# Performance work log

Measured on AMD Instinct MI355X. Metric: run time of the kernel, lower is better.

The kernel has to match this reference:

```python
import jax, jax.numpy as jnp
import numpy as np

DIM = 1024
HEADS = 16
DH = 64            # dim // heads
LOCAL_HEADS = 8
WINDOW = 128
NEG = -jnp.finfo(jnp.float32).max


def _look_around_kv(z, pad_value):
    # z: (b, h, nw, w, d) -> (b, h, nw, 3w, d); backward=1, forward=1 window
    nw = z.shape[2]
    zp = jnp.pad(z, ((0, 0), (0, 0), (1, 1), (0, 0), (0, 0)), constant_values=pad_value)
    return jnp.concatenate([zp[:, :, i:i + nw] for i in range(3)], axis=3)


def _local_attention(q, k, v, valid):
    # q,k,v: (b, h, t, d); valid: (b, t) True = keep (module passes ~input_mask)
    b, h, t, d = q.shape
    nw = t // WINDOW
    bucket = lambda z: z.reshape(b, h, nw, WINDOW, d)
    bq, bk, bv = bucket(q), bucket(k), bucket(v)
    bk = _look_around_kv(bk, 0.0)
    bv = _look_around_kv(bv, 0.0)
    # key position indices with -1 padding for out-of-range windows
    t_idx = jnp.arange(t, dtype=jnp.int32).reshape(nw, WINDOW)
    tp = jnp.pad(t_idx, ((1, 1), (0, 0)), constant_values=-1)
    bq_k = jnp.concatenate([tp[i:i + nw] for i in range(3)], axis=1)  # (nw, 3w)
    oob = (bq_k == -1)[None, None, :, None, :]                        # (1,1,nw,1,3w)
    # input mask pair: mq & mk
    vm = valid.reshape(b, nw, WINDOW)
    vmp = jnp.pad(vm, ((0, 0), (1, 1), (0, 0)), constant_values=False)
    vmk = jnp.concatenate([vmp[:, i:i + nw] for i in range(3)], axis=2)  # (b, nw, 3w)
    pair = vm[:, None, :, :, None] & vmk[:, None, :, None, :]            # (b,1,nw,w,3w)
    dots = jnp.einsum('bhnwd,bhnkd->bhnwk', bq, bk) * (d ** -0.5)
    dots = jnp.where(oob, NEG, dots)
    dots = jnp.where(pair, dots, NEG)
    attn = jax.nn.softmax(dots, axis=-1)
    out = jnp.einsum('bhnwk,bhnkd->bhnwd', attn, bv)
    return out.reshape(b, h, t, d)


def _linear_attn(q, k, v, valid):
    # q,k,v: (b, h, t, d); valid: (b, t) True = keep
    d = q.shape[-1]
    m = valid[:, None, :, None]
    k = jnp.where(m, k, NEG)
    v = jnp.where(m, v, 0.0)
    q = jax.nn.softmax(q, axis=-1) * (d ** -0.5)
    k = jax.nn.softmax(k, axis=-2)
    context = jnp.einsum('bhnd,bhne->bhde', k, v)
    return jnp.einsum('bhnd,bhde->bhne', q, context)


def setup_inputs() -> dict:
    key = jax.random.key(0)
    ks = jax.random.split(key, 7)
    b, t = 2, 4096
    x = jax.random.normal(ks[0], (b, t, DIM), dtype=jnp.float32)
    input_mask = jax.random.bernoulli(ks[1], 0.1, (b, t))  # True = padded token
    s = DIM ** -0.5
    Wq = jax.random.normal(ks[2], (DIM, HEADS * DH), jnp.float32) * s
    Wk = jax.random.normal(ks[3], (DIM, HEADS * DH), jnp.float32) * s
    Wv = jax.random.normal(ks[4], (DIM, HEADS * DH), jnp.float32) * s
    Wo = jax.random.normal(ks[5], (HEADS * DH, DIM), jnp.float32) * s
    bo = jax.random.normal(ks[6], (DIM,), jnp.float32) * 0.01
    return {"x": x, "input_mask": input_mask, "Wq": Wq, "Wk": Wk, "Wv": Wv, "Wo": Wo, "bo": bo}


def reference(x, input_mask, Wq, Wk, Wv, Wo, bo):
    b, t, _ = x.shape
    split_heads = lambda z: z.reshape(b, t, HEADS, DH).transpose(0, 2, 1, 3)
    q = split_heads(x @ Wq)
    k = split_heads(x @ Wk)
    v = split_heads(x @ Wv)
    valid = ~input_mask
    lq, gq = q[:, :LOCAL_HEADS], q[:, LOCAL_HEADS:]
    lk, gk = k[:, :LOCAL_HEADS], k[:, LOCAL_HEADS:]
    lv, gv = v[:, :LOCAL_HEADS], v[:, LOCAL_HEADS:]
    local_out = _local_attention(lq, lk, lv, valid)
    global_out = _linear_attn(gq, gk, gv, valid)
    attn = jnp.concatenate([local_out, global_out], axis=1)  # (b, h, t, d)
    attn = attn.transpose(0, 2, 1, 3).reshape(b, t, HEADS * DH)
    return attn @ Wo + bo
```

## Files before the change

kernel.cpp:

```cpp
#include <hip/hip_runtime.h>
#include <cstdint>
#include <cfloat>
#include <math.h>

typedef __bf16 bf16_t;
typedef __bf16 bf16x8 __attribute__((ext_vector_type(8)));
typedef __bf16 bf16x4 __attribute__((ext_vector_type(4)));
typedef float  f32x4  __attribute__((ext_vector_type(4)));

#define NEGF (-3.4028234663852886e38f)

static __device__ __forceinline__ f32x4 mfma16(bf16x8 a, bf16x8 b, f32x4 c) {
  return __builtin_amdgcn_mfma_f32_16x16x32_bf16(a, b, c, 0, 0, 0);
}
static __device__ __forceinline__ void gload_lds16(const bf16_t* g, bf16_t* l) {
  __builtin_amdgcn_global_load_lds((const __attribute__((address_space(1))) void*)g,
                                   (__attribute__((address_space(3))) void*)l, 16, 0, 0);
}

__global__ void k_prep(const uint8_t* __restrict__ mraw, uint8_t* __restrict__ valid) {
  __shared__ int f1, f3;
  int tid = threadIdx.x;
  if (tid == 0) { f1 = 0; f3 = 0; }
  __syncthreads();
  int l1 = 0, l3 = 0;
  for (int i = tid; i < 8192; i += 256) {
    uint8_t v = mraw[i];
    if (v) { int r = i & 3; if (r == 1 || r == 2) l1 = 1; if (r == 3) l3 = 1; }
  }
  if (l1) atomicOr(&f1, 1);
  if (l3) atomicOr(&f3, 1);
  __syncthreads();
  int layout = f1 ? 0 : (f3 ? 2 : 1);
  for (int i = tid; i < 8192; i += 256) {
    bool m;
    if (layout == 0)      m = mraw[i] != 0;
    else if (layout == 1) m = ((const int*)mraw)[i] != 0;
    else                  m = ((const float*)mraw)[i] != 0.0f;
    valid[i] = m ? (uint8_t)0 : (uint8_t)1;
  }
}

__global__ void k_cast_x(const float* __restrict__ x, bf16_t* __restrict__ xb) {
  int i = blockIdx.x * 256 + threadIdx.x;
  float4 v = ((const float4*)x)[i];
  bf16x4 o = { (bf16_t)v.x, (bf16_t)v.y, (bf16_t)v.z, (bf16_t)v.w };
  *(bf16x4*)(xb + (size_t)i * 4) = o;
}

__global__ void k_transw(const float* __restrict__ Wq, const float* __restrict__ Wk,
                         const float* __restrict__ Wv, const float* __restrict__ Wo,
                         bf16_t* __restrict__ WT, bf16_t* __restrict__ WoT) {
  __shared__ float tile[32][33];
  int z = blockIdx.z;
  const float* src = (z == 0) ? Wq : (z == 1) ? Wk : (z == 2) ? Wv : Wo;
  bf16_t* dst = (z < 3) ? (WT + (size_t)z * 1024 * 1024) : WoT;
  int x0 = blockIdx.x * 32, y0 = blockIdx.y * 32;
  int tx = threadIdx.x, ty = threadIdx.y;
  #pragma unroll
  for (int j = 0; j < 32; j += 8)
    tile[ty + j][tx] = src[(size_t)(y0 + ty + j) * 1024 + x0 + tx];
  __syncthreads();
  #pragma unroll
  for (int j = 0; j < 32; j += 8)
    dst[(size_t)(x0 + ty + j) * 1024 + y0 + tx] = (bf16_t)tile[tx][ty + j];
}

template<bool OUT_BF16>
__global__ __launch_bounds__(256, 2) void k_gemm(const bf16_t* __restrict__ A,
                                                 const bf16_t* __restrict__ Bt,
                                                 void* __restrict__ Cout,
                                                 const float* __restrict__ bias,
                                                 int M, int N, int K) {
  __shared__ __align__(16) uint8_t shmem[34816];
  bf16_t* As = (bf16_t*)shmem;
  bf16_t* Bs = As + 128 * 64;
  int nbn = N >> 7;
  int nwg = (M >> 7) * nbn;
  int per = nwg >> 3;
  int id  = blockIdx.x;
  int sw  = (id & 7) * per + (id >> 3);
  int mb = sw / nbn, nb = sw % nbn;

  const int tid = threadIdx.x;
  const int lane = tid & 63, wv = tid >> 6;
  const int c = lane & 15, g = lane >> 4;
  const size_t m0 = (size_t)mb * 128, n0 = (size_t)nb * 128;
  const int wm = (wv >> 1) * 64, wn = (wv & 1) * 64;

  f32x4 zero = {0.f, 0.f, 0.f, 0.f};
  f32x4 acc[4][4];
  #pragma unroll
  for (int m = 0; m < 4; ++m)
    #pragma unroll
    for (int n = 0; n < 4; ++n) acc[m][n] = zero;

  for (int kt = 0; kt < K; kt += 64) {
    if (kt) __syncthreads();
    #pragma unroll
    for (int p = 0; p < 4; ++p) {
      int seg = p * 256 + tid;
      int r = seg >> 3, s = seg & 7;
      int sc = (s ^ (r & 7)) * 8;
      gload_lds16(A + (m0 + r) * (size_t)K + kt + sc, As + seg * 8);
    }
    #pragma unroll
    for (int p = 0; p < 4; ++p) {
      int seg = p * 256 + tid;
      int r = seg >> 3, s = seg & 7;
      int sc = (s ^ (r & 7)) * 8;
      gload_lds16(Bt + (n0 + r) * (size_t)K + kt + sc, Bs + seg * 8);
    }
    __syncthreads();
    #pragma unroll
    for (int kk = 0; kk < 2; ++kk) {
      bf16x8 af[4], bfv[4];
      #pragma unroll
      for (int m = 0; m < 4; ++m) {
        int row = wm + m * 16 + c;
        int sl = (g + 4 * kk) ^ (row & 7);
        af[m] = *(const bf16x8*)(As + row * 64 + sl * 8);
      }
      #pragma unroll
      for (int n = 0; n < 4; ++n) {
        int row = wn + n * 16 + c;
        int sl = (g + 4 * kk) ^ (row & 7);
        bfv[n] = *(const bf16x8*)(Bs + row * 64 + sl * 8);
      }
      #pragma unroll
      for (int m = 0; m < 4; ++m)
        #pragma unroll
        for (int n = 0; n < 4; ++n)
          acc[m][n] = mfma16(af[m], bfv[n], acc[m][n]);
    }
  }

  __syncthreads();
  if (OUT_BF16) {
    bf16_t* L = (bf16_t*)shmem;
    #pragma unroll
    for (int m = 0; m < 4; ++m)
      #pragma unroll
      for (int n = 0; n < 4; ++n)
        #pragma unroll
        for (int i = 0; i < 4; ++i)
          L[(wm + m * 16 + 4 * g + i) * 136 + wn + n * 16 + c] = (bf16_t)acc[m][n][i];
    __syncthreads();
    bf16_t* C = (bf16_t*)Cout;
    #pragma unroll
    for (int p = 0; p < 8; ++p) {
      int idx = p * 2048 + tid * 8;
      int row = idx >> 7, col = idx & 127;
      bf16x8 v = *(const bf16x8*)(L + row * 136 + col);
      *(bf16x8*)(C + (m0 + row) * (size_t)N + n0 + col) = v;
    }
  } else {
    float* C = (float*)Cout;
    float* L = (float*)shmem;
    #pragma unroll
    for (int half = 0; half < 2; ++half) {
      if (half) __syncthreads();
      if ((wv >> 1) == half) {
        #pragma unroll
        for (int m = 0; m < 4; ++m)
          #pragma unroll
          for (int n = 0; n < 4; ++n)
            #pragma unroll
            for (int i = 0; i < 4; ++i)
              L[(m * 16 + 4 * g + i) * 132 + wn + n * 16 + c] = acc[m][n][i];
      }
      __syncthreads();
      #pragma unroll
      for (int p = 0; p < 8; ++p) {
        int lin = p * 1024 + tid * 4;
        int row = lin >> 7, col = lin & 127;
        float4 v = *(const float4*)(L + row * 132 + col);
        float4 bv = *(const float4*)(bias + n0 + col);
        v.x += bv.x; v.y += bv.y; v.z += bv.z; v.w += bv.w;
        *(float4*)(C + (m0 + half * 64 + row) * (size_t)N + n0 + col) = v;
      }
    }
  }
}

__global__ __launch_bounds__(512) void k_local(const bf16_t* __restrict__ qkv,
                                               const uint8_t* __restrict__ valid,
                                               bf16_t* __restrict__ attn) {
  __shared__ __align__(16) uint8_t smem[151040];
  bf16_t* Ks = (bf16_t*)smem;
  bf16_t* P  = (bf16_t*)smem;
  bf16_t* VT = (bf16_t*)(smem + 100352);
  uint8_t* s_key = smem + 150528;
  uint8_t* s_q   = smem + 150912;

  int bid = blockIdx.x;
  int w = bid & 31, h = (bid >> 5) & 7, b = bid >> 8;
  int tid = threadIdx.x;
  const int lane = tid & 63, wv = tid >> 6;
  const int c = lane & 15, g = lane >> 4;
  const int tkbase = (w - 1) * 128;

  #pragma unroll
  for (int p = 0; p < 6; ++p) {
    int seg = p * 512 + tid;
    int r = seg >> 3, s = seg & 7;
    int tk = tkbase + r;
    bf16x8 v8 = { (bf16_t)0.f,(bf16_t)0.f,(bf16_t)0.f,(bf16_t)0.f,
                  (bf16_t)0.f,(bf16_t)0.f,(bf16_t)0.f,(bf16_t)0.f };
    if ((unsigned)tk < 4096u)
      v8 = *(const bf16x8*)(qkv + (size_t)(b * 4096 + tk) * 3072 + 1024 + h * 64 + s * 8);
    *(bf16x8*)(Ks + r * 64 + ((s ^ (r & 7)) * 8)) = v8;
  }
  {
    int e = tid & 63, tg = tid >> 6;
    #pragma unroll 8
    for (int j = 0; j < 48; ++j) {
      int r = tg * 48 + j;
      int tk = tkbase + r;
      bf16_t v = (bf16_t)0.f;
      if ((unsigned)tk < 4096u)
        v = qkv[(size_t)(b * 4096 + tk) * 3072 + 2048 + h * 64 + e];
      VT[e * 392 + r] = v;
    }
  }
  if (tid < 384) {
    int tk = tkbase + tid;
    s_key[tid] = ((unsigned)tk < 4096u) ? valid[b * 4096 + tk] : (uint8_t)0;
  }
  if (tid < 128) s_q[tid] = valid[b * 4096 + w * 128 + tid];
  __syncthreads();

  int m0 = wv * 16;
  bf16x8 qa0, qa1;
  {
    const bf16_t* qrow = qkv + (size_t)(b * 4096 + w * 128 + m0 + c) * 3072 + h * 64;
    qa0 = *(const bf16x8*)(qrow + g * 8);
    qa1 = *(const bf16x8*)(qrow + 32 + g * 8);
  }
  f32x4 zero = {0.f, 0.f, 0.f, 0.f};
  f32x4 acc[24];
  #pragma unroll
  for (int nt = 0; nt < 24; ++nt) acc[nt] = zero;
  #pragma unroll
  for (int nt = 0; nt < 24; ++nt) {
    int n = nt * 16 + c;
    bf16x8 b0 = *(const bf16x8*)(Ks + n * 64 + ((g       ^ (n & 7)) * 8));
    bf16x8 b1 = *(const bf16x8*)(Ks + n * 64 + (((g + 4) ^ (n & 7)) * 8));
    acc[nt] = mfma16(qa0, b0, acc[nt]);
    acc[nt] = mfma16(qa1, b1, acc[nt]);
  }

  bool qv[4];
  #pragma unroll
  for (int i = 0; i < 4; ++i) qv[i] = s_q[m0 + 4 * g + i] != 0;
  #pragma unroll
  for (int nt = 0; nt < 24; ++nt) {
    bool kv = s_key[nt * 16 + c] != 0;
    #pragma unroll
    for (int i = 0; i < 4; ++i)
      acc[nt][i] = (kv && qv[i]) ? acc[nt][i] * 0.125f : NEGF;
  }
  float mx[4], sum[4];
  #pragma unroll
  for (int i = 0; i < 4; ++i) mx[i] = NEGF;
  #pragma unroll
  for (int nt = 0; nt < 24; ++nt)
    #pragma unroll
    for (int i = 0; i < 4; ++i) mx[i] = fmaxf(mx[i], acc[nt][i]);
  #pragma unroll
  for (int sh = 1; sh <= 8; sh <<= 1)
    #pragma unroll
    for (int i = 0; i < 4; ++i) mx[i] = fmaxf(mx[i], __shfl_xor(mx[i], sh, 64));
  #pragma unroll
  for (int i = 0; i < 4; ++i) sum[i] = 0.f;
  #pragma unroll
  for (int nt = 0; nt < 24; ++nt)
    #pragma unroll
    for (int i = 0; i < 4; ++i) {
      float e = __expf(acc[nt][i] - mx[i]);
      acc[nt][i] = e;
      sum[i] += e;
    }
  #pragma unroll
  for (int sh = 1; sh <= 8; sh <<= 1)
    #pragma unroll
    for (int i = 0; i < 4; ++i) sum[i] += __shfl_xor(sum[i], sh, 64);
  float inv[4];
  #pragma unroll
  for (int i = 0; i < 4; ++i) inv[i] = 1.f / sum[i];

  __syncthreads();
  #pragma unroll
  for (int nt = 0; nt < 24; ++nt)
    #pragma unroll
    for (int i = 0; i < 4; ++i)
      P[(m0 + 4 * g + i) * 392 + nt * 16 + c] = (bf16_t)(acc[nt][i] * inv[i]);
  __syncthreads();

  f32x4 o[4];
  #pragma unroll
  for (int n = 0; n < 4; ++n) o[n] = zero;
  #pragma unroll
  for (int ks = 0; ks < 12; ++ks) {
    bf16x8 pa = *(const bf16x8*)(P + (m0 + c) * 392 + ks * 32 + g * 8);
    #pragma unroll
    for (int n = 0; n < 4; ++n) {
      bf16x8 vb = *(const bf16x8*)(VT + (n * 16 + c) * 392 + ks * 32 + g * 8);
      o[n] = mfma16(pa, vb, o[n]);
    }
  }
  size_t obase = (size_t)(b * 4096 + w * 128 + m0) * 1024 + h * 64;
  #pragma unroll
  for (int n = 0; n < 4; ++n)
    #pragma unroll
    for (int i = 0; i < 4; ++i)
      attn[obase + (size_t)(4 * g + i) * 1024 + n * 16 + c] = (bf16_t)o[n][i];
}

__global__ __launch_bounds__(256) void k_ctx1(const bf16_t* __restrict__ qkv,
                                              const uint8_t* __restrict__ valid,
                                              float* __restrict__ ctxp,
                                              float* __restrict__ sump) {
  int bid = blockIdx.x;
  int tc = bid & 15, h = (bid >> 4) & 7, b = bid >> 7;
  int tid = threadIdx.x;
  __shared__ float sk[128][64];
  __shared__ float sv[128][64];
  float a00=0,a01=0,a02=0,a03=0,a10=0,a11=0,a12=0,a13=0;
  float a20=0,a21=0,a22=0,a23=0,a30=0,a31=0,a32=0,a33=0;
  float s0=0, s1=0, s2=0, s3=0;
  int dg = tid >> 4, eg = tid & 15;
  for (int ch = 0; ch < 2; ++ch) {
    int t0 = tc * 256 + ch * 128;
    __syncthreads();
    for (int idx = tid; idx < 1024; idx += 256) {
      int r = idx >> 3, ss = idx & 7;
      int gt = b * 4096 + t0 + r;
      bool vld = valid[gt] != 0;
      bf16x8 k8 = *(const bf16x8*)(qkv + (size_t)gt * 3072 + 1024 + (8 + h) * 64 + ss * 8);
      bf16x8 v8 = *(const bf16x8*)(qkv + (size_t)gt * 3072 + 2048 + (8 + h) * 64 + ss * 8);
      #pragma unroll
      for (int j = 0; j < 8; ++j) {
        int dd = ss * 8 + j;
        sk[r][dd] = vld ? __expf((float)k8[j]) : 0.f;
        sv[r][dd] = vld ? (float)v8[j] : 0.f;
      }
    }
    __syncthreads();
    #pragma unroll 4
    for (int r = 0; r < 128; ++r) {
      float4 a = *(const float4*)&sk[r][dg * 4];
      float4 v = *(const float4*)&sv[r][eg * 4];
      a00 += a.x*v.x; a01 += a.x*v.y; a02 += a.x*v.z; a03 += a.x*v.w;
      a10 += a.y*v.x; a11 += a.y*v.y; a12 += a.y*v.z; a13 += a.y*v.w;
      a20 += a.z*v.x; a21 += a.z*v.y; a22 += a.z*v.z; a23 += a.z*v.w;
      a30 += a.w*v.x; a31 += a.w*v.y; a32 += a.w*v.z; a33 += a.w*v.w;
      s0 += a.x; s1 += a.y; s2 += a.z; s3 += a.w;
    }
  }
  float* dst = ctxp + (size_t)((b * 8 + h) * 16 + tc) * 4096 + (dg * 4) * 64 + eg * 4;
  *(float4*)(dst + 0)   = make_float4(a00, a01, a02, a03);
  *(float4*)(dst + 64)  = make_float4(a10, a11, a12, a13);
  *(float4*)(dst + 128) = make_float4(a20, a21, a22, a23);
  *(float4*)(dst + 192) = make_float4(a30, a31, a32, a33);
  if (eg == 0)
    *(float4*)(sump + (size_t)((b * 8 + h) * 16 + tc) * 64 + dg * 4) = make_float4(s0, s1, s2, s3);
}

__global__ __launch_bounds__(256) void k_ctx2(const float* __restrict__ ctxp,
                                              const float* __restrict__ sump,
                                              bf16_t* __restrict__ ctxT) {
  int bh = blockIdx.x;
  int tid = threadIdx.x;
  __shared__ float inv[64];
  if (tid < 64) {
    float s = 0.f;
    #pragma unroll
    for (int tc = 0; tc < 16; ++tc)
      s += sump[(size_t)(bh * 16 + tc) * 64 + tid];
    inv[tid] = 1.f / s;
  }
  __syncthreads();
  for (int p = 0; p < 16; ++p) {
    int lin = p * 256 + tid;
    int d = lin >> 6, e = lin & 63;
    float s = 0.f;
    #pragma unroll
    for (int tc = 0; tc < 16; ++tc)
      s += ctxp[(size_t)(bh * 16 + tc) * 4096 + lin];
    s *= inv[d];
    ctxT[(size_t)bh * 4096 + e * 64 + d] = (bf16_t)s;
  }
}

__global__ __launch_bounds__(256) void k_linout(const bf16_t* __restrict__ qkv,
                                                const bf16_t* __restrict__ ctxT,
                                                bf16_t* __restrict__ attn) {
  int bid = blockIdx.x;
  int tb2 = bid & 15, hg = (bid >> 4) & 7, b = bid >> 7;
  int tid = threadIdx.x;
  __shared__ bf16_t qs[256 * 72];
  __shared__ bf16_t cT[64 * 72];
  {
    int t = tb2 * 256 + tid;
    const bf16_t* qrow = qkv + (size_t)(b * 4096 + t) * 3072 + (8 + hg) * 64;
    float x[64];
    #pragma unroll
    for (int s8 = 0; s8 < 8; ++s8) {
      bf16x8 q8 = *(const bf16x8*)(qrow + s8 * 8);
      #pragma unroll
      for (int j = 0; j < 8; ++j) x[s8 * 8 + j] = (float)q8[j];
    }
    float m = x[0];
    #pragma unroll
    for (int i = 1; i < 64; ++i) m = fmaxf(m, x[i]);
    float sum = 0.f;
    #pragma unroll
    for (int i = 0; i < 64; ++i) { x[i] = __expf(x[i] - m); sum += x[i]; }
    float sc = 0.125f / sum;
    #pragma unroll
    for (int s8 = 0; s8 < 8; ++s8) {
      bf16x8 o8;
      #pragma unroll
      for (int j = 0; j < 8; ++j) o8[j] = (bf16_t)(x[s8 * 8 + j] * sc);
      *(bf16x8*)(qs + tid * 72 + s8 * 8) = o8;
    }
  }
  for (int idx = tid; idx < 512; idx += 256) {
    int r = idx >> 3, s = idx & 7;
    *(bf16x8*)(cT + r * 72 + s * 8) =
      *(const bf16x8*)(ctxT + (size_t)(b * 8 + hg) * 4096 + r * 64 + s * 8);
  }
  __syncthreads();
  int lane = tid & 63, wvv = tid >> 6;
  int c = lane & 15, g = lane >> 4;
  int m0w = wvv * 64;
  f32x4 zero = {0.f, 0.f, 0.f, 0.f};
  f32x4 acc[4][4];
  #pragma unroll
  for (int m = 0; m < 4; ++m)
    #pragma unroll
    for (int n = 0; n < 4; ++n) acc[m][n] = zero;
  #pragma unroll
  for (int kk = 0; kk < 2; ++kk) {
    bf16x8 af[4], bfv[4];
    #pragma unroll
    for (int m = 0; m < 4; ++m)
      af[m] = *(const bf16x8*)(qs + (m0w + m * 16 + c) * 72 + kk * 32 + g * 8);
    #pragma unroll
    for (int n = 0; n < 4; ++n)
      bfv[n] = *(const bf16x8*)(cT + (n * 16 + c) * 72 + kk * 32 + g * 8);
    #pragma unroll
    for (int m = 0; m < 4; ++m)
      #pragma unroll
      for (int n = 0; n < 4; ++n)
        acc[m][n] = mfma16(af[m], bfv[n], acc[m][n]);
  }
  size_t obase = (size_t)(b * 4096 + tb2 * 256 + m0w) * 1024 + (8 + hg) * 64;
  #pragma unroll
  for (int m = 0; m < 4; ++m)
    #pragma unroll
    for (int n = 0; n < 4; ++n)
      #pragma unroll
      for (int i = 0; i < 4; ++i)
        attn[obase + (size_t)(m * 16 + 4 * g + i) * 1024 + n * 16 + c] = (bf16_t)acc[m][n][i];
}

extern "C" void kernel_launch(void* const* d_in, const int* in_sizes, int n_in,
                              void* d_out, int out_size, void* d_ws, size_t ws_size,
                              hipStream_t stream) {
  const float*   x    = (const float*)d_in[0];
  const uint8_t* mraw = (const uint8_t*)d_in[1];
  const float*   Wq   = (const float*)d_in[2];
  const float*   Wk   = (const float*)d_in[3];
  const float*   Wv   = (const float*)d_in[4];
  const float*   Wo   = (const float*)d_in[5];
  const float*   bo   = (const float*)d_in[6];
  uint8_t* ws = (uint8_t*)d_ws;

  uint8_t* valid = ws;
  bf16_t*  xb    = (bf16_t*)(ws + 8192);
  bf16_t*  WT    = (bf16_t*)(ws + 16785408);
  bf16_t*  WoT   = (bf16_t*)(ws + 23076864);
  bf16_t*  qkv   = (bf16_t*)(ws + 25174016);
  bf16_t*  attn  = (bf16_t*)(ws + 75505664);
  float*   ctxp  = (float*)(ws + 8192);
  float*   sump  = (float*)(ws + 4202496);
  bf16_t*  ctxT  = (bf16_t*)(ws + 4268032);

  k_prep<<<1, 256, 0, stream>>>(mraw, valid);
  k_cast_x<<<8192, 256, 0, stream>>>(x, xb);
  k_transw<<<dim3(32, 32, 4), dim3(32, 8), 0, stream>>>(Wq, Wk, Wv, Wo, WT, WoT);
  k_gemm<true><<<1536, 256, 0, stream>>>(xb, WT, (void*)qkv, nullptr, 8192, 3072, 1024);
  k_local<<<512, 512, 0, stream>>>(qkv, valid, attn);
  k_ctx1<<<256, 256, 0, stream>>>(qkv, valid, ctxp, sump);
  k_ctx2<<<16, 256, 0, stream>>>(ctxp, sump, ctxT);
  k_linout<<<256, 256, 0, stream>>>(qkv, ctxT, attn);
  k_gemm<false><<<512, 256, 0, stream>>>(attn, WoT, d_out, bo, 8192, 1024, 1024);
}
```

Before: 220.2 us.

## Keep local-attention probabilities in registers and shrink shared memory

The local attention kernel now computes S^T by swapping the MFMA operands, so each lane holds one query row's scores. The softmax reduction then needs only two cross-lane shuffles. The probabilities are moved into A-operand layout with register shuffles instead of a round trip through shared memory. Normalisation is deferred to the output write, and K and V^T share one LDS buffer. This cuts LDS from about 151KB to about 50KB, which may let more blocks run per CU. The cost is more shuffles and register pressure (12 uint4 held per lane), and the V^T load is now serialized after QK^T.

Result: no change. 218.8 us (-0.7%).

```diff
diff --git a/kernel.cpp b/kernel.cpp
--- a/kernel.cpp
+++ b/kernel.cpp
@@ -7,6 +7,7 @@
 typedef __bf16 bf16x8 __attribute__((ext_vector_type(8)));
 typedef __bf16 bf16x4 __attribute__((ext_vector_type(4)));
 typedef float  f32x4  __attribute__((ext_vector_type(4)));
+typedef unsigned int u32;
 
 #define NEGF (-3.4028234663852886e38f)
 
@@ -186,12 +187,11 @@
 __global__ __launch_bounds__(512) void k_local(const bf16_t* __restrict__ qkv,
                                                const uint8_t* __restrict__ valid,
                                                bf16_t* __restrict__ attn) {
-  __shared__ __align__(16) uint8_t smem[151040];
+  __shared__ __align__(16) uint8_t smem[50688];
   bf16_t* Ks = (bf16_t*)smem;
-  bf16_t* P  = (bf16_t*)smem;
-  bf16_t* VT = (bf16_t*)(smem + 100352);
-  uint8_t* s_key = smem + 150528;
-  uint8_t* s_q   = smem + 150912;
+  bf16_t* VT = (bf16_t*)smem;
+  uint8_t* s_key = smem + 50176;
+  uint8_t* s_q   = smem + 50560;
 
   int bid = blockIdx.x;
   int w = bid & 31, h = (bid >> 5) & 7, b = bid >> 8;
@@ -211,6 +211,34 @@
       v8 = *(const bf16x8*)(qkv + (size_t)(b * 4096 + tk) * 3072 + 1024 + h * 64 + s * 8);
     *(bf16x8*)(Ks + r * 64 + ((s ^ (r & 7)) * 8)) = v8;
   }
+  if (tid < 384) {
+    int tk = tkbase + tid;
+    s_key[tid] = ((unsigned)tk < 4096u) ? valid[b * 4096 + tk] : (uint8_t)0;
+  }
+  if (tid < 128) s_q[tid] = valid[b * 4096 + w * 128 + tid];
+  __syncthreads();
+
+  int m0 = wv * 16;
+  bf16x8 qa0, qa1;
+  {
+    const bf16_t* qrow = qkv + (size_t)(b * 4096 + w * 128 + m0 + c) * 3072 + h * 64;
+    qa0 = *(const bf16x8*)(qrow + g * 8);
+    qa1 = *(const bf16x8*)(qrow + 32 + g * 8);
+  }
+  f32x4 zero = {0.f, 0.f, 0.f, 0.f};
+  f32x4 acc[24];
+  #pragma unroll
+  for (int nt = 0; nt < 24; ++nt) acc[nt] = zero;
+  #pragma unroll
+  for (int nt = 0; nt < 24; ++nt) {
+    int n = nt * 16 + c;
+    bf16x8 k0 = *(const bf16x8*)(Ks + n * 64 + ((g       ^ (n & 7)) * 8));
+    bf16x8 k1 = *(const bf16x8*)(Ks + n * 64 + (((g + 4) ^ (n & 7)) * 8));
+    acc[nt] = mfma16(k0, qa0, acc[nt]);
+    acc[nt] = mfma16(k1, qa1, acc[nt]);
+  }
+  __syncthreads();
+
   {
     int e = tid & 63, tg = tid >> 6;
     #pragma unroll 8
@@ -223,78 +251,59 @@
       VT[e * 392 + r] = v;
     }
   }
-  if (tid < 384) {
-    int tk = tkbase + tid;
-    s_key[tid] = ((unsigned)tk < 4096u) ? valid[b * 4096 + tk] : (uint8_t)0;
-  }
-  if (tid < 128) s_q[tid] = valid[b * 4096 + w * 128 + tid];
-  __syncthreads();
-
-  int m0 = wv * 16;
-  bf16x8 qa0, qa1;
-  {
-    const bf16_t* qrow = qkv + (size_t)(b * 4096 + w * 128 + m0 + c) * 3072 + h * 64;
-    qa0 = *(const bf16x8*)(qrow + g * 8);
-    qa1 = *(const bf16x8*)(qrow + 32 + g * 8);
-  }
-  f32x4 zero = {0.f, 0.f, 0.f, 0.f};
-  f32x4 acc[24];
-  #pragma unroll
-  for (int nt = 0; nt < 24; ++nt) acc[nt] = zero;
+
+  bool qv = s_q[m0 + c] != 0;
   #pragma unroll
   for (int nt = 0; nt < 24; ++nt) {
-    int n = nt * 16 + c;
-    bf16x8 b0 = *(const bf16x8*)(Ks + n * 64 + ((g       ^ (n & 7)) * 8));
-    bf16x8 b1 = *(const bf16x8*)(Ks + n * 64 + (((g + 4) ^ (n & 7)) * 8));
-    acc[nt] = mfma16(qa0, b0, acc[nt]);
-    acc[nt] = mfma16(qa1, b1, acc[nt]);
-  }
-
-  bool qv[4];
-  #pragma unroll
-  for (int i = 0; i < 4; ++i) qv[i] = s_q[m0 + 4 * g + i] != 0;
+    u32 kv4 = *(const u32*)(s_key + nt * 16 + 4 * g);
+    #pragma unroll
+    for (int i = 0; i < 4; ++i) {
+      bool kv = ((kv4 >> (8 * i)) & 255u) != 0u;
+      acc[nt][i] = (qv && kv) ? acc[nt][i] * 0.125f : NEGF;
+    }
+  }
+  float mx = NEGF;
+  #pragma unroll
+  for (int nt = 0; nt < 24; ++nt)
+    #pragma unroll
+    for (int i = 0; i < 4; ++i) mx = fmaxf(mx, acc[nt][i]);
+  mx = fmaxf(mx, __shfl_xor(mx, 16, 64));
+  mx = fmaxf(mx, __shfl_xor(mx, 32, 64));
+
+  const int srcA = ((lane >> 4) & 1) * 32 + (lane & 15);
+  const int srcB = srcA + 16;
+  union Pk2 { bf16x4 h; uint2 u; };
+  union Pk4 { uint4 u; bf16x8 h; };
+  uint4 paU[12];
+  #pragma unroll
+  for (int ks = 0; ks < 12; ++ks) paU[ks] = make_uint4(0, 0, 0, 0);
+  float sum = 0.f;
   #pragma unroll
   for (int nt = 0; nt < 24; ++nt) {
-    bool kv = s_key[nt * 16 + c] != 0;
-    #pragma unroll
-    for (int i = 0; i < 4; ++i)
-      acc[nt][i] = (kv && qv[i]) ? acc[nt][i] * 0.125f : NEGF;
-  }
-  float mx[4], sum[4];
-  #pragma unroll
-  for (int i = 0; i < 4; ++i) mx[i] = NEGF;
-  #pragma unroll
-  for (int nt = 0; nt < 24; ++nt)
-    #pragma unroll
-    for (int i = 0; i < 4; ++i) mx[i] = fmaxf(mx[i], acc[nt][i]);
-  #pragma unroll
-  for (int sh = 1; sh <= 8; sh <<= 1)
-    #pragma unroll
-    for (int i = 0; i < 4; ++i) mx[i] = fmaxf(mx[i], __shfl_xor(mx[i], sh, 64));
-  #pragma unroll
-  for (int i = 0; i < 4; ++i) sum[i] = 0.f;
-  #pragma unroll
-  for (int nt = 0; nt < 24; ++nt)
+    Pk2 pk;
     #pragma unroll
     for (int i = 0; i < 4; ++i) {
-      float e = __expf(acc[nt][i] - mx[i]);
-      acc[nt][i] = e;
-      sum[i] += e;
-    }
-  #pragma unroll
-  for (int sh = 1; sh <= 8; sh <<= 1)
-    #pragma unroll
-    for (int i = 0; i < 4; ++i) sum[i] += __shfl_xor(sum[i], sh, 64);
-  float inv[4];
-  #pragma unroll
-  for (int i = 0; i < 4; ++i) inv[i] = 1.f / sum[i];
-
-  __syncthreads();
-  #pragma unroll
-  for (int nt = 0; nt < 24; ++nt)
-    #pragma unroll
-    for (int i = 0; i < 4; ++i)
-      P[(m0 + 4 * g + i) * 392 + nt * 16 + c] = (bf16_t)(acc[nt][i] * inv[i]);
+      float e = __expf(acc[nt][i] - mx);
+      sum += e;
+      pk.h[i] = (bf16_t)e;
+    }
+    u32 a0 = (u32)__shfl((int)pk.u.x, srcA, 64);
+    u32 a1 = (u32)__shfl((int)pk.u.y, srcA, 64);
+    u32 b0 = (u32)__shfl((int)pk.u.x, srcB, 64);
+    u32 b1 = (u32)__shfl((int)pk.u.y, srcB, 64);
+    bool take = ((g >> 1) == (nt & 1));
+    int ks = nt >> 1;
+    paU[ks].x = take ? a0 : paU[ks].x;
+    paU[ks].y = take ? a1 : paU[ks].y;
+    paU[ks].z = take ? b0 : paU[ks].z;
+    paU[ks].w = take ? b1 : paU[ks].w;
+  }
+  sum += __shfl_xor(sum, 16, 64);
+  sum += __shfl_xor(sum, 32, 64);
+  float inv = 1.f / sum;
+  float invq[4];
+  #pragma unroll
+  for (int i = 0; i < 4; ++i) invq[i] = __shfl(inv, 4 * g + i, 64);
   __syncthreads();
 
   f32x4 o[4];
@@ -302,11 +311,11 @@
   for (int n = 0; n < 4; ++n) o[n] = zero;
   #pragma unroll
   for (int ks = 0; ks < 12; ++ks) {
-    bf16x8 pa = *(const bf16x8*)(P + (m0 + c) * 392 + ks * 32 + g * 8);
+    Pk4 pa; pa.u = paU[ks];
     #pragma unroll
     for (int n = 0; n < 4; ++n) {
       bf16x8 vb = *(const bf16x8*)(VT + (n * 16 + c) * 392 + ks * 32 + g * 8);
-      o[n] = mfma16(pa, vb, o[n]);
+      o[n] = mfma16(pa.h, vb, o[n]);
     }
   }
   size_t obase = (size_t)(b * 4096 + w * 128 + m0) * 1024 + h * 64;
@@ -314,7 +323,7 @@
   for (int n = 0; n < 4; ++n)
     #pragma unroll
     for (int i = 0; i < 4; ++i)
-      attn[obase + (size_t)(4 * g + i) * 1024 + n * 16 + c] = (bf16_t)o[n][i];
+      attn[obase + (size_t)(4 * g + i) * 1024 + n * 16 + c] = (bf16_t)(o[n][i] * invq[i]);
 }
 
 __global__ __launch_bounds__(256) void k_ctx1(const bf16_t* __restrict__ qkv,
```
